# Kernel tuning notes

Hardware: AMD Instinct MI355X
Metric: run time of the kernel (lower is better)

Reference implementation:

```python
import jax, jax.numpy as jnp
import numpy as np
import math

D_MODEL = 1024
N_HEADS = 16
DEPTH = D_MODEL // N_HEADS
ROPE_BASE = 10000.0
LS_INIT = 1e-05


def _rope_cos_sin(seq_len, depth, dtype=jnp.float32):
    inv_freq = 1.0 / (ROPE_BASE ** (jnp.arange(0, depth, 2, dtype=jnp.float32) / depth))
    t = jnp.arange(seq_len, dtype=jnp.float32)
    freqs = jnp.einsum('i,j->ij', t, inv_freq)          # [S, depth/2]
    emb = jnp.concatenate([freqs, freqs], axis=-1)       # [S, depth]
    return emb.astype(dtype).cos()[None, None], emb.astype(dtype).sin()[None, None]  # wrong order fixed below


def rope_cos_sin(seq_len, depth):
    inv_freq = 1.0 / (ROPE_BASE ** (jnp.arange(0, depth, 2, dtype=jnp.float32) / depth))
    t = jnp.arange(seq_len, dtype=jnp.float32)
    freqs = jnp.einsum('i,j->ij', t, inv_freq)          # [S, depth/2]
    emb = jnp.concatenate([freqs, freqs], axis=-1)       # [S, depth]
    return jnp.cos(emb)[None, None], jnp.sin(emb)[None, None]  # [1,1,S,depth]


def rotate_half(x):
    x1, x2 = jnp.split(x, 2, axis=-1)
    return jnp.concatenate([-x2, x1], axis=-1)


def setup_inputs() -> dict:
    key = jax.random.key(0)
    ks = jax.random.split(key, 6)
    B, S, D = 2, 2048, D_MODEL
    s = 1.0 / math.sqrt(D)
    return {
        'query': jax.random.normal(ks[0], (B, S, D), dtype=jnp.float32),
        'Wq': jax.random.normal(ks[1], (D, D), dtype=jnp.float32) * s,
        'bq': jnp.zeros((D,), jnp.float32),
        'Wk': jax.random.normal(ks[2], (D, D), dtype=jnp.float32) * s,
        'bk': jnp.zeros((D,), jnp.float32),
        'Wv': jax.random.normal(ks[3], (D, D), dtype=jnp.float32) * s,
        'bv': jnp.zeros((D,), jnp.float32),
        'Wo': jax.random.normal(ks[4], (D, D), dtype=jnp.float32) * s,
        'bo': jnp.zeros((D,), jnp.float32),
        'gamma': jnp.full((D,), LS_INIT, jnp.float32),
    }


def reference(query, Wq, bq, Wk, bk, Wv, bv, Wo, bo, gamma):
    B, S, D = query.shape
    H, dh = N_HEADS, DEPTH

    def split_heads(x):  # [B,S,D] -> [B,H,S,dh]
        return x.reshape(B, S, H, dh).transpose(0, 2, 1, 3)

    # torch Linear: x @ W.T + b, W is [out,in]
    q = split_heads(query @ Wq.T + bq)
    k = split_heads(query @ Wk.T + bk)
    v = split_heads(query @ Wv.T + bv)

    cos, sin = rope_cos_sin(S, dh)  # [1,1,S,dh]
    q = q * cos + rotate_half(q) * sin
    k = k * cos + rotate_half(k) * sin

    logits = jnp.einsum('bhqd,bhkd->bhqk', q, k) / math.sqrt(dh)
    attn = jax.nn.softmax(logits, axis=-1)          # dropout = identity (eval)
    out = jnp.einsum('bhqk,bhkd->bhqd', attn, v)    # [B,H,S,dh]
    out = out.transpose(0, 2, 1, 3).reshape(B, S, D)
    out = out @ Wo.T + bo
    return gamma * out
```

## Files before the change

kernel.cpp:

```cpp
#include <hip/hip_runtime.h>
#include <hip/hip_bf16.h>
#include <math.h>

typedef __bf16 bf16_t;
typedef __bf16 bf16x8 __attribute__((ext_vector_type(8)));
typedef __bf16 bf16x4 __attribute__((ext_vector_type(4)));
typedef short short4v __attribute__((ext_vector_type(4)));
typedef float floatx4 __attribute__((ext_vector_type(4)));

#define SC_QK 0.18033688011112042f

__device__ __forceinline__ float fast_exp2(float x) {
#if __has_builtin(__builtin_amdgcn_exp2f)
  return __builtin_amdgcn_exp2f(x);
#else
  return exp2f(x);
#endif
}

__device__ __forceinline__ void async_load16(const bf16_t* g, bf16_t* l) {
  __builtin_amdgcn_global_load_lds(
      (__attribute__((address_space(1))) void*)(void*)g,
      (__attribute__((address_space(3))) void*)l, 16, 0, 0);
}

__device__ __forceinline__ void wait_and_barrier() {
  asm volatile("" ::: "memory");
  __builtin_amdgcn_s_waitcnt(0x0070);
  __builtin_amdgcn_s_barrier();
  asm volatile("" ::: "memory");
}

__device__ __forceinline__ floatx4 mfma_pv(bf16x4 vfrag, bf16x4 pfrag,
                                           floatx4 acc) {
#if __has_builtin(__builtin_amdgcn_mfma_f32_16x16x16bf16_1k)
  return __builtin_amdgcn_mfma_f32_16x16x16bf16_1k(
      __builtin_bit_cast(short4v, vfrag), __builtin_bit_cast(short4v, pfrag),
      acc, 0, 0, 0);
#else
  const bf16_t z = (bf16_t)0.0f;
  bf16x8 a = {vfrag[0], vfrag[1], vfrag[2], vfrag[3], z, z, z, z};
  bf16x8 b = {pfrag[0], pfrag[1], pfrag[2], pfrag[3], z, z, z, z};
  return __builtin_amdgcn_mfma_f32_16x16x32_bf16(a, b, acc, 0, 0, 0);
#endif
}

__global__ __launch_bounds__(256) void convert_kernel(
    const float* __restrict__ query, const float* __restrict__ Wq,
    const float* __restrict__ Wk, const float* __restrict__ Wv,
    const float* __restrict__ Wo, bf16_t* __restrict__ Xbf,
    bf16_t* __restrict__ Wqkv, bf16_t* __restrict__ Wobf,
    float* __restrict__ tab) {
  if (blockIdx.x >= 8192) {
    int idx = (blockIdx.x - 8192) * 256 + threadIdx.x;
    int s = idx >> 5;
    int p = idx & 31;
    float invf = __expf(-(float)p * 0.28782313662425576f);
    float ang = (float)s * invf;
    float c, sn;
    sincosf(ang, &sn, &c);
    tab[idx] = c;
    tab[65536 + idx] = sn;
    return;
  }
  long base = ((long)blockIdx.x * 256 + threadIdx.x) * 4;
  const float* src;
  bf16_t* dst;
  long off;
  if (base < 4194304L)      { src = query; dst = Xbf;             off = base; }
  else if (base < 5242880L) { src = Wq;    dst = Wqkv;            off = base - 4194304L; }
  else if (base < 6291456L) { src = Wk;    dst = Wqkv + 1048576;  off = base - 5242880L; }
  else if (base < 7340032L) { src = Wv;    dst = Wqkv + 2097152;  off = base - 6291456L; }
  else                      { src = Wo;    dst = Wobf;            off = base - 7340032L; }
  float4 v = *reinterpret_cast<const float4*>(src + off);
  dst[off + 0] = (bf16_t)v.x;
  dst[off + 1] = (bf16_t)v.y;
  dst[off + 2] = (bf16_t)v.z;
  dst[off + 3] = (bf16_t)v.w;
}

__device__ __forceinline__ void gemm_tile_db(const bf16_t* __restrict__ A,
                                             const bf16_t* __restrict__ Bn,
                                             int m0, int n0,
                                             floatx4 acc[4][4]) {
  __shared__ __align__(16) bf16_t As[2][4096];
  __shared__ __align__(16) bf16_t Bs[2][4096];
  const int tid = threadIdx.x;
  const int lane = tid & 63;
  const int wave = tid >> 6;
  const int wm = (wave >> 1) * 64;
  const int wn = (wave & 1) * 64;
  const int lr = lane & 15;
  const int lq = lane >> 4;
  const int srow = lane >> 2;
  const int scol = (lane & 3) * 8;

  auto stage = [&](int kk, int p) {
#pragma unroll
    for (int u = 0; u < 2; u++) {
      int t = wave * 2 + u;
      int row = t * 16 + srow;
      async_load16(A + (size_t)(m0 + row) * 1024 + kk + scol, &As[p][t * 512]);
      async_load16(Bn + (size_t)(n0 + row) * 1024 + kk + scol, &Bs[p][t * 512]);
    }
  };

  stage(0, 0);
  for (int it = 0; it < 32; it++) {
    const int p = it & 1;
    wait_and_barrier();
    if (it < 31) stage((it + 1) * 32, p ^ 1);
    bf16x8 af[4], bfr[4];
#pragma unroll
    for (int i = 0; i < 4; i++)
      af[i] = *reinterpret_cast<const bf16x8*>(&As[p][(wm + i * 16 + lr) * 32 + lq * 8]);
#pragma unroll
    for (int j = 0; j < 4; j++)
      bfr[j] = *reinterpret_cast<const bf16x8*>(&Bs[p][(wn + j * 16 + lr) * 32 + lq * 8]);
#pragma unroll
    for (int i = 0; i < 4; i++)
#pragma unroll
      for (int j = 0; j < 4; j++)
        acc[i][j] = __builtin_amdgcn_mfma_f32_16x16x32_bf16(af[i], bfr[j],
                                                            acc[i][j], 0, 0, 0);
  }
}

__global__ __launch_bounds__(256, 3) void qkv_kernel(
    const bf16_t* __restrict__ Xbf, const bf16_t* __restrict__ Wqkv,
    const float* __restrict__ bq, const float* __restrict__ bk,
    const float* __restrict__ bv, const float* __restrict__ Tab,
    bf16_t* __restrict__ Qbuf, bf16_t* __restrict__ Kbuf,
    bf16_t* __restrict__ Vt) {
  const int m0 = blockIdx.x * 128;
  const int n0 = blockIdx.y * 128;
  const int z = blockIdx.z;
  floatx4 acc[4][4];
  floatx4 zero4 = {0.f, 0.f, 0.f, 0.f};
#pragma unroll
  for (int i = 0; i < 4; i++)
#pragma unroll
    for (int j = 0; j < 4; j++) acc[i][j] = zero4;

  gemm_tile_db(Xbf, Wqkv + (size_t)z * 1048576, m0, n0, acc);

  const int lane = threadIdx.x & 63;
  const int wave = threadIdx.x >> 6;
  const int wm = (wave >> 1) * 64;
  const int wn = (wave & 1) * 64;
  const int lr = lane & 15;
  const int lq = lane >> 4;
  const int h = (n0 + wn) >> 6;

  if (z == 2) {
    const int b = m0 >> 11;
    const int sbase = (m0 & 2047) + wm + lq * 4;
#pragma unroll
    for (int i = 0; i < 4; i++)
#pragma unroll
      for (int j = 0; j < 4; j++) {
        int n = n0 + wn + j * 16 + lr;
        int d = j * 16 + lr;
        float bias = bv[n];
        bf16x4 pk;
#pragma unroll
        for (int r = 0; r < 4; r++) pk[r] = (bf16_t)(acc[i][j][r] + bias);
        *reinterpret_cast<bf16x4*>(
            &Vt[((size_t)(b * 16 + h) * 64 + d) * 2048 + sbase + i * 16]) = pk;
      }
  } else {
    bf16_t* dst = (z == 0) ? Qbuf : Kbuf;
    const float* bias = (z == 0) ? bq : bk;
    const float sc = (z == 0) ? SC_QK : 1.0f;
#pragma unroll
    for (int i = 0; i < 4; i++)
#pragma unroll
      for (int r = 0; r < 4; r++) {
        int m = m0 + wm + i * 16 + lq * 4 + r;
        int b = m >> 11, s = m & 2047;
        size_t rowbase = ((size_t)(b * 16 + h) * 2048 + s) * 64;
#pragma unroll
        for (int jj = 0; jj < 2; jj++) {
          int d1 = jj * 16 + lr;
          int n1 = n0 + wn + d1;
          float x1 = acc[i][jj][r] + bias[n1];
          float x2 = acc[i][jj + 2][r] + bias[n1 + 32];
          float c = Tab[s * 32 + d1];
          float sn = Tab[65536 + s * 32 + d1];
          dst[rowbase + d1]      = (bf16_t)((x1 * c - x2 * sn) * sc);
          dst[rowbase + d1 + 32] = (bf16_t)((x2 * c + x1 * sn) * sc);
        }
      }
  }
}

__global__ __launch_bounds__(512, 2) void attn_kernel(
    const bf16_t* __restrict__ Qbuf, const bf16_t* __restrict__ Kbuf,
    const bf16_t* __restrict__ Vt, bf16_t* __restrict__ Ctx) {
  __shared__ __align__(16) bf16_t Sh[2][16384];
  const int tid = threadIdx.x;
  const int lane = tid & 63;
  const int w = tid >> 6;
  const int lr = lane & 15;
  const int lq = lane >> 4;
  const int q0 = blockIdx.x * 256;
  const int bh = blockIdx.y;
  const size_t hb = (size_t)bh * (2048 * 64);
  const int qw = q0 + w * 32;

  bf16x8 qf[2][2];
#pragma unroll
  for (int g = 0; g < 2; g++) {
    const bf16_t* qp = Qbuf + hb + (size_t)(qw + g * 16 + lr) * 64 + lq * 8;
    qf[g][0] = *reinterpret_cast<const bf16x8*>(qp);
    qf[g][1] = *reinterpret_cast<const bf16x8*>(qp + 32);
  }

  floatx4 o[2][4];
  floatx4 lsum4[2];
  floatx4 zero4 = {0.f, 0.f, 0.f, 0.f};
#pragma unroll
  for (int g = 0; g < 2; g++) {
    lsum4[g] = zero4;
#pragma unroll
    for (int dt = 0; dt < 4; dt++) o[g][dt] = zero4;
  }

  const int ksr = lane >> 3;
  const int ksb = lane & 7;
  const int vsr = lane >> 4;
  const int vsb = lane & 15;

  auto stage = [&](int kt, int p) {
    const int k0 = kt * 128;
    bf16_t* Ks = Sh[p];
    bf16_t* Vs = Sh[p] + 8192;
#pragma unroll
    for (int u = 0; u < 2; u++) {
      int t = w * 2 + u;
      {
        int r = t * 8 + ksr;
        int c = ksb ^ (r & 7);
        async_load16(Kbuf + hb + (size_t)(k0 + r) * 64 + c * 8, Ks + t * 512);
      }
      {
        int d = t * 4 + vsr;
        int c = vsb ^ (d & 15);
        async_load16(Vt + hb + (size_t)d * 2048 + k0 + c * 8, Vs + t * 512);
      }
    }
  };

  stage(0, 0);

  for (int kt = 0; kt < 16; kt++) {
    const int p = kt & 1;
    const bf16_t* Ks = Sh[p];
    const bf16_t* Vs = Sh[p] + 8192;

    wait_and_barrier();
    if (kt < 15) stage(kt + 1, p ^ 1);

    bf16x4 pg[2][8];
#pragma unroll
    for (int nt = 0; nt < 8; nt++) {
      int krow = nt * 16 + lr;
      bf16x8 kf0 = *reinterpret_cast<const bf16x8*>(
          &Ks[krow * 64 + (lq ^ (krow & 7)) * 8]);
      bf16x8 kf1 = *reinterpret_cast<const bf16x8*>(
          &Ks[krow * 64 + ((4 + lq) ^ (krow & 7)) * 8]);
#pragma unroll
      for (int g = 0; g < 2; g++) {
        floatx4 z4 = zero4;
        z4 = __builtin_amdgcn_mfma_f32_16x16x32_bf16(kf0, qf[g][0], z4, 0, 0, 0);
        z4 = __builtin_amdgcn_mfma_f32_16x16x32_bf16(kf1, qf[g][1], z4, 0, 0, 0);
#pragma unroll
        for (int r = 0; r < 4; r++) {
          float pv = fast_exp2(z4[r]);
          lsum4[g][r] += pv;
          pg[g][nt][r] = (bf16_t)pv;
        }
      }
    }

#pragma unroll
    for (int nt = 0; nt < 8; nt++) {
      bf16x4 vf[4];
#pragma unroll
      for (int dt = 0; dt < 4; dt++) {
        int d = dt * 16 + lr;
        int blk = (2 * nt + (lq >> 1)) ^ (d & 15);
        vf[dt] = *reinterpret_cast<const bf16x4*>(
            &Vs[d * 128 + blk * 8 + (lq & 1) * 4]);
      }
#pragma unroll
      for (int g = 0; g < 2; g++)
#pragma unroll
        for (int dt = 0; dt < 4; dt++)
          o[g][dt] = mfma_pv(vf[dt], pg[g][nt], o[g][dt]);
    }
  }

  const int b = bh >> 4;
  const int h = bh & 15;
#pragma unroll
  for (int g = 0; g < 2; g++) {
    float l = (lsum4[g][0] + lsum4[g][1]) + (lsum4[g][2] + lsum4[g][3]);
    l += __shfl_xor(l, 16, 64);
    l += __shfl_xor(l, 32, 64);
    float inv_l = 1.0f / l;
    size_t rowb = ((size_t)(b * 2048 + qw + g * 16 + lr)) * 1024 + h * 64;
#pragma unroll
    for (int dt = 0; dt < 4; dt++) {
      bf16x4 pk;
#pragma unroll
      for (int r = 0; r < 4; r++) pk[r] = (bf16_t)(o[g][dt][r] * inv_l);
      *reinterpret_cast<bf16x4*>(&Ctx[rowb + dt * 16 + lq * 4]) = pk;
    }
  }
}

__global__ __launch_bounds__(256, 2) void oproj_kernel(
    const bf16_t* __restrict__ Ctx, const bf16_t* __restrict__ Wobf,
    const float* __restrict__ bo, const float* __restrict__ gamma,
    float* __restrict__ out) {
  __shared__ __align__(16) bf16_t As[2][2048];
  __shared__ __align__(16) bf16_t Bs[2][4096];
  const int m0 = blockIdx.x * 64;
  const int n0 = blockIdx.y * 128;
  const int tid = threadIdx.x;
  const int lane = tid & 63;
  const int wave = tid >> 6;
  const int wn = wave * 32;
  const int lr = lane & 15;
  const int lq = lane >> 4;
  const int srow = lane >> 2;
  const int scol = (lane & 3) * 8;

  floatx4 acc[4][2];
  floatx4 zero4 = {0.f, 0.f, 0.f, 0.f};
#pragma unroll
  for (int i = 0; i < 4; i++)
#pragma unroll
    for (int j = 0; j < 2; j++) acc[i][j] = zero4;

  auto stage = [&](int kk, int p) {
    {
      int row = wave * 16 + srow;
      async_load16(Ctx + (size_t)(m0 + row) * 1024 + kk + scol,
                   &As[p][wave * 512]);
    }
#pragma unroll
    for (int u = 0; u < 2; u++) {
      int t = wave * 2 + u;
      int row = t * 16 + srow;
      async_load16(Wobf + (size_t)(n0 + row) * 1024 + kk + scol,
                   &Bs[p][t * 512]);
    }
  };

  stage(0, 0);
  for (int it = 0; it < 32; it++) {
    const int p = it & 1;
    wait_and_barrier();
    if (it < 31) stage((it + 1) * 32, p ^ 1);
    bf16x8 af[4], bfr[2];
#pragma unroll
    for (int i = 0; i < 4; i++)
      af[i] = *reinterpret_cast<const bf16x8*>(&As[p][(i * 16 + lr) * 32 + lq * 8]);
#pragma unroll
    for (int j = 0; j < 2; j++)
      bfr[j] = *reinterpret_cast<const bf16x8*>(&Bs[p][(wn + j * 16 + lr) * 32 + lq * 8]);
#pragma unroll
    for (int i = 0; i < 4; i++)
#pragma unroll
      for (int j = 0; j < 2; j++)
        acc[i][j] = __builtin_amdgcn_mfma_f32_16x16x32_bf16(af[i], bfr[j],
                                                            acc[i][j], 0, 0, 0);
  }

#pragma unroll
  for (int i = 0; i < 4; i++)
#pragma unroll
    for (int j = 0; j < 2; j++)
#pragma unroll
      for (int r = 0; r < 4; r++) {
        int m = m0 + i * 16 + lq * 4 + r;
        int n = n0 + wn + j * 16 + lr;
        out[(size_t)m * 1024 + n] = gamma[n] * (acc[i][j][r] + bo[n]);
      }
}

extern "C" void kernel_launch(void* const* d_in, const int* in_sizes, int n_in,
                              void* d_out, int out_size, void* d_ws,
                              size_t ws_size, hipStream_t stream) {
  const float* query = (const float*)d_in[0];
  const float* Wq = (const float*)d_in[1];
  const float* bq = (const float*)d_in[2];
  const float* Wk = (const float*)d_in[3];
  const float* bk = (const float*)d_in[4];
  const float* Wv = (const float*)d_in[5];
  const float* bv = (const float*)d_in[6];
  const float* Wo = (const float*)d_in[7];
  const float* bo = (const float*)d_in[8];
  const float* gamma = (const float*)d_in[9];
  float* out = (float*)d_out;

  char* ws = (char*)d_ws;
  bf16_t* Xbf  = (bf16_t*)(ws);
  bf16_t* Wqkv = (bf16_t*)(ws + (8ull << 20));
  bf16_t* Wobf = (bf16_t*)(ws + (14ull << 20));
  bf16_t* Qbuf = (bf16_t*)(ws + (16ull << 20));
  bf16_t* Kbuf = (bf16_t*)(ws + (24ull << 20));
  bf16_t* Vt   = (bf16_t*)(ws + (32ull << 20));
  bf16_t* Ctx  = (bf16_t*)(ws + (40ull << 20));
  float*  Tab  = (float*)(ws + (40ull << 20));

  convert_kernel<<<dim3(8448), dim3(256), 0, stream>>>(query, Wq, Wk, Wv, Wo,
                                                       Xbf, Wqkv, Wobf, Tab);
  qkv_kernel<<<dim3(32, 8, 3), dim3(256), 0, stream>>>(Xbf, Wqkv, bq, bk, bv,
                                                       Tab, Qbuf, Kbuf, Vt);
  attn_kernel<<<dim3(8, 32), dim3(512), 0, stream>>>(Qbuf, Kbuf, Vt, Ctx);
  oproj_kernel<<<dim3(64, 8), dim3(256), 0, stream>>>(Ctx, Wobf, bo, gamma, out);
}
```

Baseline: 198.0 us.

## Switch GEMM and attention loops to triple-buffered async LDS pipelines

Moves the QKV GEMM, output projection and attention K/V staging from double to triple buffering, prefetching two stages ahead. Partial vmcnt waits let the next tile's loads stay in flight across the barrier. Attention K/V tiles shrink from 128 to 64 keys, with the V swizzle adjusted to match, so the three buffers still fit. The convert kernel now writes a packed bf16x4 store instead of four scalar stores. The cost is more LDS per block in the GEMMs, which may lower occupancy, and twice as many barriers in the attention loop.

```diff
diff --git a/kernel.cpp b/kernel.cpp
--- a/kernel.cpp
+++ b/kernel.cpp
@@ -24,12 +24,13 @@
       (__attribute__((address_space(3))) void*)l, 16, 0, 0);
 }
 
-__device__ __forceinline__ void wait_and_barrier() {
-  asm volatile("" ::: "memory");
-  __builtin_amdgcn_s_waitcnt(0x0070);
-  __builtin_amdgcn_s_barrier();
-  asm volatile("" ::: "memory");
-}
+#define WAITB(imm)                       \
+  do {                                   \
+    asm volatile("" ::: "memory");       \
+    __builtin_amdgcn_s_waitcnt(imm);     \
+    __builtin_amdgcn_s_barrier();        \
+    asm volatile("" ::: "memory");       \
+  } while (0)
 
 __device__ __forceinline__ floatx4 mfma_pv(bf16x4 vfrag, bf16x4 pfrag,
                                            floatx4 acc) {
@@ -73,18 +74,16 @@
   else if (base < 7340032L) { src = Wv;    dst = Wqkv + 2097152;  off = base - 6291456L; }
   else                      { src = Wo;    dst = Wobf;            off = base - 7340032L; }
   float4 v = *reinterpret_cast<const float4*>(src + off);
-  dst[off + 0] = (bf16_t)v.x;
-  dst[off + 1] = (bf16_t)v.y;
-  dst[off + 2] = (bf16_t)v.z;
-  dst[off + 3] = (bf16_t)v.w;
-}
-
-__device__ __forceinline__ void gemm_tile_db(const bf16_t* __restrict__ A,
-                                             const bf16_t* __restrict__ Bn,
-                                             int m0, int n0,
-                                             floatx4 acc[4][4]) {
-  __shared__ __align__(16) bf16_t As[2][4096];
-  __shared__ __align__(16) bf16_t Bs[2][4096];
+  bf16x4 pk = {(bf16_t)v.x, (bf16_t)v.y, (bf16_t)v.z, (bf16_t)v.w};
+  *reinterpret_cast<bf16x4*>(dst + off) = pk;
+}
+
+__device__ __forceinline__ void gemm_tile_db3(const bf16_t* __restrict__ A,
+                                              const bf16_t* __restrict__ Bn,
+                                              int m0, int n0,
+                                              floatx4 acc[4][4]) {
+  __shared__ __align__(16) bf16_t As[3][4096];
+  __shared__ __align__(16) bf16_t Bs[3][4096];
   const int tid = threadIdx.x;
   const int lane = tid & 63;
   const int wave = tid >> 6;
@@ -106,10 +105,11 @@
   };
 
   stage(0, 0);
+  stage(32, 1);
   for (int it = 0; it < 32; it++) {
-    const int p = it & 1;
-    wait_and_barrier();
-    if (it < 31) stage((it + 1) * 32, p ^ 1);
+    const int p = it % 3;
+    if (it == 31) WAITB(0x0070); else WAITB(0x0074);
+    if (it < 30) stage((it + 2) * 32, (it + 2) % 3);
     bf16x8 af[4], bfr[4];
 #pragma unroll
     for (int i = 0; i < 4; i++)
@@ -142,7 +142,7 @@
 #pragma unroll
     for (int j = 0; j < 4; j++) acc[i][j] = zero4;
 
-  gemm_tile_db(Xbf, Wqkv + (size_t)z * 1048576, m0, n0, acc);
+  gemm_tile_db3(Xbf, Wqkv + (size_t)z * 1048576, m0, n0, acc);
 
   const int lane = threadIdx.x & 63;
   const int wave = threadIdx.x >> 6;
@@ -197,7 +197,7 @@
 __global__ __launch_bounds__(512, 2) void attn_kernel(
     const bf16_t* __restrict__ Qbuf, const bf16_t* __restrict__ Kbuf,
     const bf16_t* __restrict__ Vt, bf16_t* __restrict__ Ctx) {
-  __shared__ __align__(16) bf16_t Sh[2][16384];
+  __shared__ __align__(16) bf16_t Sh[3][8192];
   const int tid = threadIdx.x;
   const int lane = tid & 63;
   const int w = tid >> 6;
@@ -226,44 +226,39 @@
     for (int dt = 0; dt < 4; dt++) o[g][dt] = zero4;
   }
 
-  const int ksr = lane >> 3;
-  const int ksb = lane & 7;
-  const int vsr = lane >> 4;
-  const int vsb = lane & 15;
+  const int sr = lane >> 3;
+  const int sb = lane & 7;
 
   auto stage = [&](int kt, int p) {
-    const int k0 = kt * 128;
+    const int k0 = kt * 64;
     bf16_t* Ks = Sh[p];
-    bf16_t* Vs = Sh[p] + 8192;
-#pragma unroll
-    for (int u = 0; u < 2; u++) {
-      int t = w * 2 + u;
-      {
-        int r = t * 8 + ksr;
-        int c = ksb ^ (r & 7);
-        async_load16(Kbuf + hb + (size_t)(k0 + r) * 64 + c * 8, Ks + t * 512);
-      }
-      {
-        int d = t * 4 + vsr;
-        int c = vsb ^ (d & 15);
-        async_load16(Vt + hb + (size_t)d * 2048 + k0 + c * 8, Vs + t * 512);
-      }
+    bf16_t* Vs = Sh[p] + 4096;
+    {
+      int r = w * 8 + sr;
+      int c = sb ^ (r & 7);
+      async_load16(Kbuf + hb + (size_t)(k0 + r) * 64 + c * 8, Ks + w * 512);
+    }
+    {
+      int d = w * 8 + sr;
+      int c = sb ^ (d & 7);
+      async_load16(Vt + hb + (size_t)d * 2048 + k0 + c * 8, Vs + w * 512);
     }
   };
 
   stage(0, 0);
-
-  for (int kt = 0; kt < 16; kt++) {
-    const int p = kt & 1;
+  stage(1, 1);
+
+  for (int kt = 0; kt < 32; kt++) {
+    const int p = kt % 3;
     const bf16_t* Ks = Sh[p];
-    const bf16_t* Vs = Sh[p] + 8192;
-
-    wait_and_barrier();
-    if (kt < 15) stage(kt + 1, p ^ 1);
-
-    bf16x4 pg[2][8];
-#pragma unroll
-    for (int nt = 0; nt < 8; nt++) {
+    const bf16_t* Vs = Sh[p] + 4096;
+
+    if (kt == 31) WAITB(0x0070); else WAITB(0x0072);
+    if (kt < 30) stage(kt + 2, (kt + 2) % 3);
+
+    bf16x4 pg[2][4];
+#pragma unroll
+    for (int nt = 0; nt < 4; nt++) {
       int krow = nt * 16 + lr;
       bf16x8 kf0 = *reinterpret_cast<const bf16x8*>(
           &Ks[krow * 64 + (lq ^ (krow & 7)) * 8]);
@@ -284,14 +279,14 @@
     }
 
 #pragma unroll
-    for (int nt = 0; nt < 8; nt++) {
+    for (int nt = 0; nt < 4; nt++) {
       bf16x4 vf[4];
 #pragma unroll
       for (int dt = 0; dt < 4; dt++) {
         int d = dt * 16 + lr;
-        int blk = (2 * nt + (lq >> 1)) ^ (d & 15);
+        int blk = (2 * nt + (lq >> 1)) ^ (d & 7);
         vf[dt] = *reinterpret_cast<const bf16x4*>(
-            &Vs[d * 128 + blk * 8 + (lq & 1) * 4]);
+            &Vs[d * 64 + blk * 8 + (lq & 1) * 4]);
       }
 #pragma unroll
       for (int g = 0; g < 2; g++)
@@ -324,8 +319,8 @@
     const bf16_t* __restrict__ Ctx, const bf16_t* __restrict__ Wobf,
     const float* __restrict__ bo, const float* __restrict__ gamma,
     float* __restrict__ out) {
-  __shared__ __align__(16) bf16_t As[2][2048];
-  __shared__ __align__(16) bf16_t Bs[2][4096];
+  __shared__ __align__(16) bf16_t As[3][2048];
+  __shared__ __align__(16) bf16_t Bs[3][4096];
   const int m0 = blockIdx.x * 64;
   const int n0 = blockIdx.y * 128;
   const int tid = threadIdx.x;
@@ -360,10 +355,11 @@
   };
 
   stage(0, 0);
+  stage(32, 1);
   for (int it = 0; it < 32; it++) {
-    const int p = it & 1;
-    wait_and_barrier();
-    if (it < 31) stage((it + 1) * 32, p ^ 1);
+    const int p = it % 3;
+    if (it == 31) WAITB(0x0070); else WAITB(0x0073);
+    if (it < 30) stage((it + 2) * 32, (it + 2) % 3);
     bf16x8 af[4], bfr[2];
 #pragma unroll
     for (int i = 0; i < 4; i++)
```

Result: no change. 198.8 us (+0.4%).
